# Kernel optimization log

Hardware: AMD Instinct MI355X
Metric: run time of the kernel (lower is better)

Reference implementation:

```python
import jax, jax.numpy as jnp
import numpy as np

NEG_INF = -1e30  # masked_softmax fill (squad util convention)


def setup_inputs() -> dict:
    key = jax.random.key(0)
    ks = jax.random.split(key, 5)
    B, S, H = 4, 2048, 512
    x = jax.random.normal(ks[0], (B, S, H), dtype=jnp.float32)
    mask = jax.random.randint(ks[1], (B, S), 0, 2, dtype=jnp.int32)
    mask = mask.at[:, 0].set(1)  # ensure at least one valid key per row
    W_comb = jax.random.normal(ks[2], (H, 3 * H), dtype=jnp.float32) * (1.0 / np.sqrt(H))
    b_comb = jnp.zeros((3 * H,), dtype=jnp.float32)
    W_out = jax.random.normal(ks[3], (H, H), dtype=jnp.float32) * (1.0 / np.sqrt(H))
    b_out = jnp.zeros((H,), dtype=jnp.float32)
    return {"x": x, "mask": mask, "W_comb": W_comb, "b_comb": b_comb,
            "W_out": W_out, "b_out": b_out}


def reference(x, mask, W_comb, b_comb, W_out, b_out):
    B, S, H = x.shape
    n_head = 8
    d = H // n_head
    scale = d ** 0.5
    qkv = x @ W_comb + b_comb                      # [B,S,3H]
    q, k, v = jnp.split(qkv, 3, axis=-1)
    q = q.reshape(B, S, n_head, d)
    k = k.reshape(B, S, n_head, d)
    v = v.reshape(B, S, n_head, d)
    # [B,h,Sq,Sk] scores; mask applies along the key axis
    scores = jnp.einsum('bqhd,bkhd->bhqk', q / scale, k)
    key_mask = (mask > 0)[:, None, None, :]        # [B,1,1,Sk]
    logits = jnp.where(key_mask, scores, NEG_INF)
    attn = jax.nn.softmax(logits, axis=-1)         # dropout = identity (eval)
    out = jnp.einsum('bhqk,bkhd->bqhd', attn, v).reshape(B, S, H)
    return out @ W_out + b_out
```

## Files before the change

kernel.cpp:

```cpp
#include <hip/hip_runtime.h>
#include <hip/hip_bf16.h>
#include <stdint.h>

typedef unsigned short u16;
typedef unsigned int u32;
typedef __attribute__((ext_vector_type(8))) __bf16 bf16x8;
typedef __attribute__((ext_vector_type(8))) unsigned short us8;
typedef __attribute__((ext_vector_type(4))) unsigned short us4;
typedef __attribute__((ext_vector_type(4))) float f32x4;
typedef __attribute__((ext_vector_type(16))) float f32x16;
typedef __attribute__((ext_vector_type(4))) unsigned int u32x4;
typedef __attribute__((ext_vector_type(2))) unsigned int u32x2;

#define KSCALE_Q 0.18033688011112042f

#define VMCNT(n) asm volatile("s_waitcnt vmcnt(" #n ")" ::: "memory")
#define BARRIER() __builtin_amdgcn_s_barrier()

__device__ inline u16 f2bf(float f) {
  union { __bf16 b; u16 s; } x; x.b = (__bf16)f; return x.s;
}
__device__ inline u32 packbf(float a, float b) {
  return (u32)f2bf(a) | ((u32)f2bf(b) << 16);
}
__device__ inline f32x16 zero16() {
  f32x16 z; for (int i = 0; i < 16; ++i) z[i] = 0.f; return z;
}
__device__ __forceinline__ void gl_lds16(const u16* g, u16* l) {
  __builtin_amdgcn_global_load_lds(
      (const __attribute__((address_space(1))) void*)g,
      (__attribute__((address_space(3))) void*)l, 16, 0, 0);
}
__device__ __forceinline__ void pl32swap(u32& a, u32& b) {
#if __has_builtin(__builtin_amdgcn_permlane32_swap)
  u32x2 r = __builtin_amdgcn_permlane32_swap(a, b, false, false);
  a = r[0]; b = r[1];
#else
  u32 ta = (u32)__shfl_xor((int)a, 32);
  u32 tb = (u32)__shfl_xor((int)b, 32);
  int hi = (threadIdx.x & 63) >> 5;
  u32 na = hi ? tb : a;
  u32 nb = hi ? b : ta;
  a = na; b = nb;
#endif
}

__global__ __launch_bounds__(256) void prep(
    const float* __restrict__ x, const float* __restrict__ Wc,
    const float* __restrict__ Wo, const int* __restrict__ mask,
    u16* __restrict__ xbf, u16* __restrict__ wct, u16* __restrict__ wot,
    int* __restrict__ idx, int* __restrict__ nbv) {
  int r = blockIdx.x, tid = threadIdx.x;
  if (r < 4096) {
    int i = r * 256 + tid;
    float4 v = ((const float4*)x)[i];
    us4 o;
    o[0] = f2bf(v.x); o[1] = f2bf(v.y); o[2] = f2bf(v.z); o[3] = f2bf(v.w);
    ((us4*)xbf)[i] = o;
    return;
  }
  __shared__ float tile[32][33];
  __shared__ int ps[256];
  if (r < 5120) {
    const float* in; u16* outT; int R, C, bi;
    if (r < 4864) { in = Wc; outT = wct; R = 512; C = 1536; bi = r - 4096; }
    else          { in = Wo; outT = wot; R = 512; C = 512;  bi = r - 4864; }
    int nbx = C >> 5;
    int bx = bi % nbx, by = bi / nbx;
    int xq = tid & 31, yq = tid >> 5;
    int c0 = bx * 32, r0 = by * 32;
    for (int j = 0; j < 32; j += 8)
      tile[yq + j][xq] = in[(size_t)(r0 + yq + j) * C + c0 + xq];
    __syncthreads();
    for (int j = 0; j < 32; j += 8)
      outT[(size_t)(c0 + yq + j) * R + r0 + xq] = f2bf(tile[xq][yq + j]);
    return;
  }
  int b = r - 5120;
  const int* mrow = mask + b * 2048;
  int4 a = ((const int4*)mrow)[tid * 2];
  int4 c = ((const int4*)mrow)[tid * 2 + 1];
  int v[8] = {a.x, a.y, a.z, a.w, c.x, c.y, c.z, c.w};
  int cnt = 0;
  for (int i = 0; i < 8; ++i) cnt += (v[i] > 0);
  ps[tid] = cnt;
  __syncthreads();
  for (int off = 1; off < 256; off <<= 1) {
    int xv = ps[tid];
    int yv = (tid >= off) ? ps[tid - off] : 0;
    __syncthreads();
    ps[tid] = xv + yv;
    __syncthreads();
  }
  int total = ps[255];
  int pos = ps[tid] - cnt;
  int* ip = idx + b * 2048;
  for (int i = 0; i < 8; ++i)
    if (v[i] > 0) ip[pos++] = tid * 8 + i;
  for (int i = 0; i < 8; ++i) {
    int j = tid * 8 + i;
    if (j >= total) ip[j] = 0;
  }
  if (tid == 0) nbv[b] = total;
}

__global__ __launch_bounds__(256) void gemm_qkv(
    const u16* __restrict__ A, const u16* __restrict__ Bt,
    const float* __restrict__ bias, u16* __restrict__ Qc,
    u16* __restrict__ Kc, u16* __restrict__ VTc,
    const int* __restrict__ idx, const int* __restrict__ nbv) {
  const int K = 512;
  int bid = blockIdx.x;
  bool isQ = bid < 256;
  int b = 0, m0, n0;
  if (isQ) {
    m0 = (bid >> 2) * 128;
    n0 = (bid & 3) * 128;
  } else {
    int t = bid - 256;
    b = t >> 7;
    int rr_ = t & 127;
    m0 = (rr_ & 15) * 128;
    n0 = (rr_ >> 4) * 128 + 512;
    int npad = (nbv[b] + 127) & ~127;
    if (m0 >= npad) return;
  }
  __shared__ __align__(16) u16 As[2][128 * 64];
  __shared__ __align__(16) u16 Bs[2][128 * 64];
  int tid = threadIdx.x, wave = tid >> 6, lane = tid & 63;
  int quad = lane >> 4, l16 = lane & 15;
  int wm = (wave >> 1) * 64, wn = (wave & 1) * 64;

  int r8 = lane >> 3;
  int cb = (lane & 7) ^ r8;
  const u16* agp[4];
  for (int i = 0; i < 4; ++i) {
    int row = m0 + wave * 32 + i * 8 + r8;
    int grow = isQ ? row : (b * 2048 + idx[b * 2048 + row]);
    agp[i] = A + (size_t)grow * K + cb * 8;
  }
  const u16* bg = Bt + (size_t)(n0 + wave * 32 + r8) * K + cb * 8;
  int lofs = (wave * 32) * 64 + lane * 8;

  f32x4 acc[4][4];
  for (int i = 0; i < 4; ++i)
    for (int j = 0; j < 4; ++j) acc[i][j] = (f32x4){0.f, 0.f, 0.f, 0.f};

  int rx = l16 & 7;

  auto stage = [&](int buf, int kk) {
    u16* al = As[buf] + lofs;
    u16* bl = Bs[buf] + lofs;
#pragma unroll
    for (int i = 0; i < 4; ++i)
      gl_lds16(agp[i] + kk, al + i * 8 * 64);
#pragma unroll
    for (int i = 0; i < 4; ++i)
      gl_lds16(bg + kk + (size_t)(i * 8) * K, bl + i * 8 * 64);
  };

  stage(0, 0);
  for (int t = 0; t < 8; ++t) {
    if (t < 7) { stage((t + 1) & 1, (t + 1) * 64); VMCNT(8); }
    else       { VMCNT(0); }
    BARRIER();
    const u16* Asb = As[t & 1];
    const u16* Bsb = Bs[t & 1];
#pragma unroll
    for (int ks = 0; ks < 2; ++ks) {
      int pos = ((ks * 4 + quad) ^ rx) * 8;
      bf16x8 af[4], bfr[4];
#pragma unroll
      for (int i = 0; i < 4; ++i)
        af[i] = *(const bf16x8*)(Asb + (wm + i * 16 + l16) * 64 + pos);
#pragma unroll
      for (int j = 0; j < 4; ++j)
        bfr[j] = *(const bf16x8*)(Bsb + (wn + j * 16 + l16) * 64 + pos);
#pragma unroll
      for (int i = 0; i < 4; ++i)
#pragma unroll
        for (int j = 0; j < 4; ++j)
          acc[i][j] = __builtin_amdgcn_mfma_f32_16x16x32_bf16(
              af[i], bfr[j], acc[i][j], 0, 0, 0);
    }
    BARRIER();
  }
  for (int j = 0; j < 4; ++j) {
    int col = n0 + wn + j * 16 + l16;
    float bv = bias[col];
    if (isQ) {
      for (int i = 0; i < 4; ++i) {
        int rowb = m0 + wm + i * 16 + quad * 4;
        for (int rr = 0; rr < 4; ++rr)
          Qc[(size_t)(rowb + rr) * 512 + col] =
              f2bf((acc[i][j][rr] + bv) * KSCALE_Q);
      }
    } else if (col < 1024) {
      int ck = col - 512;
      for (int i = 0; i < 4; ++i) {
        int key0 = m0 + wm + i * 16 + quad * 4;
        for (int rr = 0; rr < 4; ++rr)
          Kc[((size_t)b * 2048 + key0 + rr) * 512 + ck] =
              f2bf(acc[i][j][rr] + bv);
      }
    } else {
      int hd = col - 1024;
      int h = hd >> 6, d = hd & 63;
      u16* vrow = VTc + ((size_t)(b * 8 + h) * 64 + d) * 2048;
      for (int i = 0; i < 4; ++i) {
        int key0 = m0 + wm + i * 16 + quad * 4;
        us4 pk;
        for (int rr = 0; rr < 4; ++rr) pk[rr] = f2bf(acc[i][j][rr] + bv);
        *(us4*)(vrow + key0) = pk;
      }
    }
  }
}

__global__ __launch_bounds__(256) void gemm_out(
    const u16* __restrict__ A, const u16* __restrict__ Bt,
    const float* __restrict__ bias, float* __restrict__ Cout) {
  const int K = 512, N = 512;
  int m0 = blockIdx.y * 128, n0 = blockIdx.x * 128;
  __shared__ __align__(16) u16 As[2][128 * 64];
  __shared__ __align__(16) u16 Bs[2][128 * 64];
  int tid = threadIdx.x, wave = tid >> 6, lane = tid & 63;
  int quad = lane >> 4, l16 = lane & 15;
  int wm = (wave >> 1) * 64, wn = (wave & 1) * 64;

  int r8 = lane >> 3;
  int cb = (lane & 7) ^ r8;
  const u16* ag = A + (size_t)(m0 + wave * 32 + r8) * K + cb * 8;
  const u16* bg = Bt + (size_t)(n0 + wave * 32 + r8) * K + cb * 8;
  int lofs = (wave * 32) * 64 + lane * 8;

  f32x4 acc[4][4];
  for (int i = 0; i < 4; ++i)
    for (int j = 0; j < 4; ++j) acc[i][j] = (f32x4){0.f, 0.f, 0.f, 0.f};

  int rx = l16 & 7;

  auto stage = [&](int buf, int kk) {
    u16* al = As[buf] + lofs;
    u16* bl = Bs[buf] + lofs;
#pragma unroll
    for (int i = 0; i < 4; ++i)
      gl_lds16(ag + kk + (size_t)(i * 8) * K, al + i * 8 * 64);
#pragma unroll
    for (int i = 0; i < 4; ++i)
      gl_lds16(bg + kk + (size_t)(i * 8) * K, bl + i * 8 * 64);
  };

  stage(0, 0);
  for (int t = 0; t < 8; ++t) {
    if (t < 7) { stage((t + 1) & 1, (t + 1) * 64); VMCNT(8); }
    else       { VMCNT(0); }
    BARRIER();
    const u16* Asb = As[t & 1];
    const u16* Bsb = Bs[t & 1];
#pragma unroll
    for (int ks = 0; ks < 2; ++ks) {
      int pos = ((ks * 4 + quad) ^ rx) * 8;
      bf16x8 af[4], bfr[4];
#pragma unroll
      for (int i = 0; i < 4; ++i)
        af[i] = *(const bf16x8*)(Asb + (wm + i * 16 + l16) * 64 + pos);
#pragma unroll
      for (int j = 0; j < 4; ++j)
        bfr[j] = *(const bf16x8*)(Bsb + (wn + j * 16 + l16) * 64 + pos);
#pragma unroll
      for (int i = 0; i < 4; ++i)
#pragma unroll
        for (int j = 0; j < 4; ++j)
          acc[i][j] = __builtin_amdgcn_mfma_f32_16x16x32_bf16(
              af[i], bfr[j], acc[i][j], 0, 0, 0);
    }
    BARRIER();
  }
  for (int j = 0; j < 4; ++j) {
    int col = n0 + wn + j * 16 + l16;
    float bv = bias[col];
    for (int i = 0; i < 4; ++i) {
      int rowb = m0 + wm + i * 16 + quad * 4;
      for (int rr = 0; rr < 4; ++rr)
        Cout[(size_t)(rowb + rr) * N + col] = acc[i][j][rr] + bv;
    }
  }
}

__global__ __launch_bounds__(256, 2) void attn_kernel(
    const u16* __restrict__ Qc, const u16* __restrict__ Kc,
    const u16* __restrict__ VTc, const int* __restrict__ nbv,
    u16* __restrict__ aout) {
  int flat = blockIdx.x;
  int xcd = flat & 7, ii = flat >> 3;
  int p = ((ii >> 4) << 3) | xcd;
  int c = ii & 15;
  int b = p >> 3, h = p & 7, q0 = c * 128;
  int bh = b * 8 + h;
  int tid = threadIdx.x, wave = tid >> 6, lane = tid & 63;
  int l5 = lane & 31, hi = lane >> 5;
  int nb = nbv[b];
  int npad = (nb + 127) & ~127;
  int NT = npad >> 7;

  __shared__ __align__(16) u16 Kt[2][128 * 64];
  __shared__ __align__(16) u16 Vt[2][64 * 128];

  bf16x8 qf[4];
  int qrow = b * 2048 + q0 + wave * 32 + l5;
#pragma unroll
  for (int s = 0; s < 4; ++s)
    qf[s] = *(const bf16x8*)(Qc + (size_t)qrow * 512 + h * 64 + s * 16 +
                             hi * 8);
  VMCNT(0);

  f32x16 o[2];
  o[0] = zero16(); o[1] = zero16();
  float lsum = 0.f;

  int krr = lane >> 3;
  int kcb = (lane & 7) ^ krr;
  const u16* kg = Kc + ((size_t)(b * 2048) + wave * 32 + krr) * 512 + h * 64 +
                  kcb * 8;
  int vrr = lane >> 4;

  auto stageKV = [&](int buf, int kt0) {
    u16* kl = Kt[buf] + (wave * 32) * 64 + lane * 8;
#pragma unroll
    for (int i = 0; i < 4; ++i)
      gl_lds16(kg + (size_t)(kt0 + i * 8) * 512, kl + i * 8 * 64);
    u16* vl = Vt[buf] + (wave * 16) * 128 + lane * 8;
#pragma unroll
    for (int i = 0; i < 4; ++i) {
      int vr = wave * 16 + i * 4 + vrr;
      int vcb = (lane & 15) ^ (vr & 15);
      gl_lds16(VTc + ((size_t)(bh * 64) + vr) * 2048 + kt0 + vcb * 8,
               vl + i * 4 * 128);
    }
  };

  int rx = l5 & 7;
  stageKV(0, 0);
  for (int t = 0; t < NT; ++t) {
    if (t + 1 < NT) { stageKV((t + 1) & 1, (t + 1) * 128); VMCNT(8); }
    else            { VMCNT(0); }
    BARRIER();
    const u16* Ktc = Kt[t & 1];
    const u16* Vtc = Vt[t & 1];
    int kt0 = t * 128;
    bool maskT = (kt0 + 128 > nb);

#pragma unroll
    for (int kp = 0; kp < 2; ++kp) {
      bf16x8 ka[2][4];
#pragma unroll
      for (int cc = 0; cc < 2; ++cc) {
        const u16* kro = Ktc + ((kp * 2 + cc) * 32 + l5) * 64;
#pragma unroll
        for (int s = 0; s < 4; ++s)
          ka[cc][s] = *(const bf16x8*)(kro + ((s * 2 + hi) ^ rx) * 8);
      }
      f32x16 sa[2];
      sa[0] = zero16(); sa[1] = zero16();
#pragma unroll
      for (int s = 0; s < 4; ++s) {
        sa[0] = __builtin_amdgcn_mfma_f32_32x32x16_bf16(ka[0][s], qf[s],
                                                        sa[0], 0, 0, 0);
        sa[1] = __builtin_amdgcn_mfma_f32_32x32x16_bf16(ka[1][s], qf[s],
                                                        sa[1], 0, 0, 0);
      }
      bf16x8 pb[2][2];
#pragma unroll
      for (int cc = 0; cc < 2; ++cc) {
        int kg4 = kp * 2 + cc;
        if (maskT) {
#pragma unroll
          for (int r = 0; r < 16; ++r) {
            int jg = kt0 + kg4 * 32 + (r & 3) + 8 * (r >> 2) + 4 * hi;
            if (jg >= nb) sa[cc][r] = -1e30f;
          }
        }
        u32 pk[8];
        float ls = 0.f;
#pragma unroll
        for (int j = 0; j < 8; ++j) {
          float e0 = __builtin_amdgcn_exp2f(sa[cc][2 * j]);
          float e1 = __builtin_amdgcn_exp2f(sa[cc][2 * j + 1]);
          ls += e0 + e1;
          pk[j] = packbf(e0, e1);
        }
        lsum += ls;
#pragma unroll
        for (int t2 = 0; t2 < 2; ++t2) {
          u32 a0 = pk[t2 * 4 + 0], a2 = pk[t2 * 4 + 2];
          u32 a1 = pk[t2 * 4 + 1], a3 = pk[t2 * 4 + 3];
          pl32swap(a0, a2);
          pl32swap(a1, a3);
          u32x4 qv; qv[0] = a0; qv[1] = a1; qv[2] = a2; qv[3] = a3;
          pb[cc][t2] = __builtin_bit_cast(bf16x8, qv);
        }
      }
#pragma unroll
      for (int cc = 0; cc < 2; ++cc) {
        int kg4 = kp * 2 + cc;
#pragma unroll
        for (int t2 = 0; t2 < 2; ++t2) {
          int cblk = kg4 * 4 + t2 * 2 + hi;
#pragma unroll
          for (int dc = 0; dc < 2; ++dc) {
            int vrow = dc * 32 + l5;
            bf16x8 va = *(const bf16x8*)(Vtc + vrow * 128 +
                                         ((cblk ^ (vrow & 15)) * 8));
            o[dc] = __builtin_amdgcn_mfma_f32_32x32x16_bf16(
                va, pb[cc][t2], o[dc], 0, 0, 0);
          }
        }
      }
    }
    BARRIER();
  }

  float lt = lsum;
  lt += __shfl_xor(lt, 32);
  float inv = 1.f / lt;
#pragma unroll
  for (int dc = 0; dc < 2; ++dc)
#pragma unroll
    for (int mI = 0; mI < 4; ++mI) {
      us4 pk;
      for (int r = 0; r < 4; ++r) pk[r] = f2bf(o[dc][mI * 4 + r] * inv);
      *(us4*)(aout + (size_t)qrow * 512 + h * 64 + dc * 32 + mI * 8 +
              hi * 4) = pk;
    }
}

extern "C" void kernel_launch(void* const* d_in, const int* in_sizes, int n_in,
                              void* d_out, int out_size, void* d_ws,
                              size_t ws_size, hipStream_t stream) {
  const float* x = (const float*)d_in[0];
  const int* mask = (const int*)d_in[1];
  const float* Wc = (const float*)d_in[2];
  const float* bc = (const float*)d_in[3];
  const float* Wo = (const float*)d_in[4];
  const float* bo = (const float*)d_in[5];
  float* out = (float*)d_out;

  char* ws = (char*)d_ws;
  u16* xbf = (u16*)(ws);
  u16* wct = (u16*)(ws + 8388608);
  u16* wot = (u16*)(ws + 9961472);
  u16* Qc  = (u16*)(ws + 10485760);
  u16* Kc  = (u16*)(ws + 18874368);
  u16* vtc = (u16*)(ws + 27262976);
  int* idx = (int*)(ws + 35651584);
  int* nbv = (int*)(ws + 35684352);
  u16* aout = xbf;

  prep<<<5124, 256, 0, stream>>>(x, Wc, Wo, mask, xbf, wct, wot, idx, nbv);
  gemm_qkv<<<768, 256, 0, stream>>>(xbf, wct, bc, Qc, Kc, vtc, idx, nbv);
  attn_kernel<<<512, 256, 0, stream>>>(Qc, Kc, vtc, nbv, aout);
  gemm_out<<<dim3(4, 64), 256, 0, stream>>>(aout, wot, bo, out);
}
```

Baseline: 144.2 us.

## Coarsen prep conversion, XCD-aware GEMM block mapping, narrower out-GEMM tiles, MFMA priority hints

The x-to-bf16 conversion now handles eight float4 chunks per thread with fewer blocks. Both GEMMs remap block ids so consecutive blocks on the same XCD share A rows, which should improve L2 reuse. The output GEMM moves to 128x64 tiles over 512 blocks with a launch_bounds occupancy hint, giving more parallelism. The attention kernel raises wave priority around its MFMA sections with s_setprio. The main risk is more redundant A loads from the narrower output tiles.

```diff
diff --git a/kernel.cpp b/kernel.cpp
--- a/kernel.cpp
+++ b/kernel.cpp
@@ -5,7 +5,6 @@
 typedef unsigned short u16;
 typedef unsigned int u32;
 typedef __attribute__((ext_vector_type(8))) __bf16 bf16x8;
-typedef __attribute__((ext_vector_type(8))) unsigned short us8;
 typedef __attribute__((ext_vector_type(4))) unsigned short us4;
 typedef __attribute__((ext_vector_type(4))) float f32x4;
 typedef __attribute__((ext_vector_type(16))) float f32x16;
@@ -51,20 +50,23 @@
     u16* __restrict__ xbf, u16* __restrict__ wct, u16* __restrict__ wot,
     int* __restrict__ idx, int* __restrict__ nbv) {
   int r = blockIdx.x, tid = threadIdx.x;
-  if (r < 4096) {
-    int i = r * 256 + tid;
-    float4 v = ((const float4*)x)[i];
-    us4 o;
-    o[0] = f2bf(v.x); o[1] = f2bf(v.y); o[2] = f2bf(v.z); o[3] = f2bf(v.w);
-    ((us4*)xbf)[i] = o;
+  if (r < 512) {
+#pragma unroll
+    for (int t = 0; t < 8; ++t) {
+      int i = (r * 8 + t) * 256 + tid;
+      float4 v = ((const float4*)x)[i];
+      us4 o;
+      o[0] = f2bf(v.x); o[1] = f2bf(v.y); o[2] = f2bf(v.z); o[3] = f2bf(v.w);
+      ((us4*)xbf)[i] = o;
+    }
     return;
   }
   __shared__ float tile[32][33];
   __shared__ int ps[256];
-  if (r < 5120) {
+  if (r < 1536) {
     const float* in; u16* outT; int R, C, bi;
-    if (r < 4864) { in = Wc; outT = wct; R = 512; C = 1536; bi = r - 4096; }
-    else          { in = Wo; outT = wot; R = 512; C = 512;  bi = r - 4864; }
+    if (r < 1280) { in = Wc; outT = wct; R = 512; C = 1536; bi = r - 512; }
+    else          { in = Wo; outT = wot; R = 512; C = 512;  bi = r - 1280; }
     int nbx = C >> 5;
     int bx = bi % nbx, by = bi / nbx;
     int xq = tid & 31, yq = tid >> 5;
@@ -76,7 +78,7 @@
       outT[(size_t)(c0 + yq + j) * R + r0 + xq] = f2bf(tile[xq][yq + j]);
     return;
   }
-  int b = r - 5120;
+  int b = r - 1536;
   const int* mrow = mask + b * 2048;
   int4 a = ((const int4*)mrow)[tid * 2];
   int4 c = ((const int4*)mrow)[tid * 2 + 1];
@@ -114,14 +116,16 @@
   bool isQ = bid < 256;
   int b = 0, m0, n0;
   if (isQ) {
-    m0 = (bid >> 2) * 128;
-    n0 = (bid & 3) * 128;
+    int xcd = bid & 7, i = bid >> 3;
+    m0 = (xcd * 8 + (i >> 2)) * 128;
+    n0 = (i & 3) * 128;
   } else {
     int t = bid - 256;
-    b = t >> 7;
-    int rr_ = t & 127;
-    m0 = (rr_ & 15) * 128;
-    n0 = (rr_ >> 4) * 128 + 512;
+    int xcd = t & 7, i = t >> 3;
+    int bm = xcd + (i >> 3) * 8;
+    b = bm >> 4;
+    m0 = (bm & 15) * 128;
+    n0 = (i & 7) * 128 + 512;
     int npad = (nbv[b] + 127) & ~127;
     if (m0 >= npad) return;
   }
@@ -217,43 +221,47 @@
   }
 }
 
-__global__ __launch_bounds__(256) void gemm_out(
+__global__ __launch_bounds__(256, 3) void gemm_out(
     const u16* __restrict__ A, const u16* __restrict__ Bt,
     const float* __restrict__ bias, float* __restrict__ Cout) {
   const int K = 512, N = 512;
-  int m0 = blockIdx.y * 128, n0 = blockIdx.x * 128;
+  int bid = blockIdx.x;
+  int xcd = bid & 7, i0 = bid >> 3;
+  int m0 = (xcd * 8 + (i0 >> 3)) * 128;
+  int n0 = (i0 & 7) * 64;
   __shared__ __align__(16) u16 As[2][128 * 64];
-  __shared__ __align__(16) u16 Bs[2][128 * 64];
+  __shared__ __align__(16) u16 Bs[2][64 * 64];
   int tid = threadIdx.x, wave = tid >> 6, lane = tid & 63;
   int quad = lane >> 4, l16 = lane & 15;
-  int wm = (wave >> 1) * 64, wn = (wave & 1) * 64;
+  int wm = (wave >> 1) * 64, wn = (wave & 1) * 32;
 
   int r8 = lane >> 3;
   int cb = (lane & 7) ^ r8;
   const u16* ag = A + (size_t)(m0 + wave * 32 + r8) * K + cb * 8;
-  const u16* bg = Bt + (size_t)(n0 + wave * 32 + r8) * K + cb * 8;
-  int lofs = (wave * 32) * 64 + lane * 8;
-
-  f32x4 acc[4][4];
+  const u16* bg = Bt + (size_t)(n0 + wave * 16 + r8) * K + cb * 8;
+  int lofsA = (wave * 32) * 64 + lane * 8;
+  int lofsB = (wave * 16) * 64 + lane * 8;
+
+  f32x4 acc[4][2];
   for (int i = 0; i < 4; ++i)
-    for (int j = 0; j < 4; ++j) acc[i][j] = (f32x4){0.f, 0.f, 0.f, 0.f};
+    for (int j = 0; j < 2; ++j) acc[i][j] = (f32x4){0.f, 0.f, 0.f, 0.f};
 
   int rx = l16 & 7;
 
   auto stage = [&](int buf, int kk) {
-    u16* al = As[buf] + lofs;
-    u16* bl = Bs[buf] + lofs;
+    u16* al = As[buf] + lofsA;
+    u16* bl = Bs[buf] + lofsB;
 #pragma unroll
     for (int i = 0; i < 4; ++i)
       gl_lds16(ag + kk + (size_t)(i * 8) * K, al + i * 8 * 64);
 #pragma unroll
-    for (int i = 0; i < 4; ++i)
+    for (int i = 0; i < 2; ++i)
       gl_lds16(bg + kk + (size_t)(i * 8) * K, bl + i * 8 * 64);
   };
 
   stage(0, 0);
   for (int t = 0; t < 8; ++t) {
-    if (t < 7) { stage((t + 1) & 1, (t + 1) * 64); VMCNT(8); }
+    if (t < 7) { stage((t + 1) & 1, (t + 1) * 64); VMCNT(6); }
     else       { VMCNT(0); }
     BARRIER();
     const u16* Asb = As[t & 1];
@@ -261,23 +269,23 @@
 #pragma unroll
     for (int ks = 0; ks < 2; ++ks) {
       int pos = ((ks * 4 + quad) ^ rx) * 8;
-      bf16x8 af[4], bfr[4];
+      bf16x8 af[4], bfr[2];
 #pragma unroll
       for (int i = 0; i < 4; ++i)
         af[i] = *(const bf16x8*)(Asb + (wm + i * 16 + l16) * 64 + pos);
 #pragma unroll
-      for (int j = 0; j < 4; ++j)
+      for (int j = 0; j < 2; ++j)
         bfr[j] = *(const bf16x8*)(Bsb + (wn + j * 16 + l16) * 64 + pos);
 #pragma unroll
       for (int i = 0; i < 4; ++i)
 #pragma unroll
-        for (int j = 0; j < 4; ++j)
+        for (int j = 0; j < 2; ++j)
           acc[i][j] = __builtin_amdgcn_mfma_f32_16x16x32_bf16(
               af[i], bfr[j], acc[i][j], 0, 0, 0);
     }
     BARRIER();
   }
-  for (int j = 0; j < 4; ++j) {
+  for (int j = 0; j < 2; ++j) {
     int col = n0 + wn + j * 16 + l16;
     float bv = bias[col];
     for (int i = 0; i < 4; ++i) {
@@ -363,6 +371,7 @@
       }
       f32x16 sa[2];
       sa[0] = zero16(); sa[1] = zero16();
+      __builtin_amdgcn_s_setprio(1);
 #pragma unroll
       for (int s = 0; s < 4; ++s) {
         sa[0] = __builtin_amdgcn_mfma_f32_32x32x16_bf16(ka[0][s], qf[s],
@@ -370,6 +379,7 @@
         sa[1] = __builtin_amdgcn_mfma_f32_32x32x16_bf16(ka[1][s], qf[s],
                                                         sa[1], 0, 0, 0);
       }
+      __builtin_amdgcn_s_setprio(0);
       bf16x8 pb[2][2];
 #pragma unroll
       for (int cc = 0; cc < 2; ++cc) {
@@ -401,6 +411,7 @@
           pb[cc][t2] = __builtin_bit_cast(bf16x8, qv);
         }
       }
+      __builtin_amdgcn_s_setprio(1);
 #pragma unroll
       for (int cc = 0; cc < 2; ++cc) {
         int kg4 = kp * 2 + cc;
@@ -417,6 +428,7 @@
           }
         }
       }
+      __builtin_amdgcn_s_setprio(0);
     }
     BARRIER();
   }
@@ -457,8 +469,8 @@
   int* nbv = (int*)(ws + 35684352);
   u16* aout = xbf;
 
-  prep<<<5124, 256, 0, stream>>>(x, Wc, Wo, mask, xbf, wct, wot, idx, nbv);
+  prep<<<1540, 256, 0, stream>>>(x, Wc, Wo, mask, xbf, wct, wot, idx, nbv);
   gemm_qkv<<<768, 256, 0, stream>>>(xbf, wct, bc, Qc, Kc, vtc, idx, nbv);
   attn_kernel<<<512, 256, 0, stream>>>(Qc, Kc, vtc, nbv, aout);
-  gemm_out<<<dim3(4, 64), 256, 0, stream>>>(aout, wot, bo, out);
-}
+  gemm_out<<<512, 256, 0, stream>>>(aout, wot, bo, out);
+}
```

After: 140.8 us (median of 3 runs). -2.4%, faster.
